# Performance work log

Measured on AMD Instinct MI355X. Metric: run time of the kernel, lower is better.

Reference implementation:

```python
import jax, jax.numpy as jnp
import numpy as np

B, T, D = 4, 2048, 1024
RANK, FACTOR, SUB = 8, 64, 4
S = 4 * SUB  # 16


def construct_hamilton(A):
    # A: [rank, 4, sub, sub] -> [rank, 4*sub, 4*sub]
    r, i, j, k = A[:, 0], A[:, 1], A[:, 2], A[:, 3]
    return jnp.concatenate([
        jnp.concatenate([r, -i, -j, -k], axis=2),
        jnp.concatenate([i, r, -k, j], axis=2),
        jnp.concatenate([j, k, r, -i], axis=2),
        jnp.concatenate([k, -j, i, r], axis=2),
    ], axis=1)


def setup_inputs() -> dict:
    key = jax.random.key(0)
    k1, k2, k3 = jax.random.split(key, 3)
    x = jax.random.normal(k1, (B, T, D), dtype=jnp.float32)
    A = jax.random.normal(k2, (RANK, 4, SUB, SUB), dtype=jnp.float32)
    # orthogonal-ish init with (r+1)^-0.5 scaling, like the torch init
    fB = jax.random.normal(k3, (RANK, FACTOR, FACTOR), dtype=jnp.float32)
    q, _ = jnp.linalg.qr(fB)
    scale = (jnp.arange(RANK, dtype=jnp.float32) + 1.0) ** -0.5
    factors_B = q * scale[:, None, None]
    bias = jnp.zeros((D,), dtype=jnp.float32)
    return {"x": x, "A": A, "factors_B": factors_B, "bias": bias}


def reference(x, A, factors_B, bias):
    Bb, Tt, Dd = x.shape
    x_flat = x.reshape(-1, S, FACTOR)          # [N, s, i]
    H = construct_hamilton(A)                   # [r, k, s]
    wav = jnp.einsum('nsi,rji->rnsj', x_flat, factors_B)  # [r, N, s, j]
    out = jnp.einsum('rnsj,rks->nkj', wav, H)   # [N, k, j]
    return out.reshape(Bb, Tt, Dd) + bias
```

## Files before the change

### kernel.cpp

```cpp
#include <hip/hip_runtime.h>
#include <stdint.h>

#define RANKS 8
#define MDIM 8192
#define KDIM 1024
#define NDIM 1024
#define BM 128
#define BN 128
#define BK 32
#define NT (KDIM / BK)
#define THREADS 256

typedef __bf16 bf16x8 __attribute__((ext_vector_type(8)));
typedef float f32x4  __attribute__((ext_vector_type(4)));
typedef float f32x16 __attribute__((ext_vector_type(16)));

__device__ __forceinline__ unsigned short f2bf(float f) {
  union { float f; uint32_t u; } v; v.f = f;
  uint32_t u = v.u;
  u += 0x7FFFu + ((u >> 16) & 1u);
  return (unsigned short)(u >> 16);
}

__constant__ int   c_comp[4][4] = {{0,1,2,3},{1,0,3,2},{2,3,0,1},{3,2,1,0}};
__constant__ float c_sign[4][4] = {{1.f,-1.f,-1.f,-1.f},
                                   {1.f, 1.f,-1.f, 1.f},
                                   {1.f, 1.f, 1.f,-1.f},
                                   {1.f,-1.f, 1.f, 1.f}};

__global__ void build_W(const float* __restrict__ A, const float* __restrict__ fB,
                        unsigned short* __restrict__ W) {
  int idx = blockIdx.x * 256 + threadIdx.x;
  int p  = idx >> 8;
  int q4 = (idx & 255) << 2;
  int k = p >> 6, j = p & 63;
  int kb = k >> 2, ks = k & 3;
  int s = q4 >> 6;
  int sb = s >> 2, ss = s & 3;
  int   comp = c_comp[kb][sb];
  float sgn  = c_sign[kb][sb];
  float o0 = 0.f, o1 = 0.f, o2 = 0.f, o3 = 0.f;
  int i0 = q4 & 63;
#pragma unroll
  for (int r = 0; r < RANKS; ++r) {
    float h = sgn * A[r * 64 + comp * 16 + ks * 4 + ss];
    const float* fb = fB + r * 4096 + j * 64 + i0;
    o0 += h * fb[0]; o1 += h * fb[1]; o2 += h * fb[2]; o3 += h * fb[3];
  }
  ushort4 st;
  st.x = f2bf(o0); st.y = f2bf(o1); st.z = f2bf(o2); st.w = f2bf(o3);
  *reinterpret_cast<ushort4*>(W + (size_t)p * KDIM + q4) = st;
}

__device__ __forceinline__ void gload16(const void* g, void* l) {
  __builtin_amdgcn_global_load_lds(
      (const __attribute__((address_space(1))) unsigned int*)(uintptr_t)g,
      (__attribute__((address_space(3))) unsigned int*)(uintptr_t)l,
      16, 0, 0);
}

__global__ __launch_bounds__(THREADS, 3) void gemm_ham(
    const float* __restrict__ x, const unsigned short* __restrict__ W,
    const float* __restrict__ bias, float* __restrict__ out) {
  __shared__ float          Asm_[2][BM * BK];
  __shared__ unsigned short Bsm_[2][BN * BK];

  const int tid  = threadIdx.x;
  const int lane = tid & 63;
  const int wid  = tid >> 6;
  const int wr   = wid >> 1;
  const int wc   = wid & 1;
  const int l31  = lane & 31;
  const int g    = lane >> 5;

  const int flat = blockIdx.x;
  const int xg = flat & 7, ig = flat >> 3;
  const int bx = xg * 8 + (ig >> 3);
  const int by = ig & 7;
  const int row0 = bx * BM;
  const int col0 = by * BN;

  f32x16 acc[2][2];
#pragma unroll
  for (int m = 0; m < 2; ++m)
#pragma unroll
    for (int n = 0; n < 2; ++n)
#pragma unroll
      for (int v = 0; v < 16; ++v) acc[m][n][v] = 0.f;

  auto stageA = [&](int kt, int slot) {
#pragma unroll
    for (int gg = 0; gg < 4; ++gg) {
      int id = gg * 256 + tid;
      int r = id >> 3, ct = id & 7;
      gload16(x + (size_t)(row0 + r) * KDIM + kt * BK + ((ct ^ (r & 7)) << 2),
              &Asm_[slot][id * 4]);
    }
  };
  auto stageB = [&](int kt, int slot) {
#pragma unroll
    for (int gg = 0; gg < 2; ++gg) {
      int id = gg * 256 + tid;
      int r = id >> 2, ct = id & 3;
      gload16(W + (size_t)(col0 + r) * KDIM + kt * BK + ((ct ^ ((r >> 1) & 3)) << 3),
              &Bsm_[slot][id * 8]);
    }
  };

  stageA(0, 0); stageB(0, 0);
  __syncthreads();

  int cur = 0;
#pragma unroll 1
  for (int t = 0; t < NT; ++t) {
    if (t + 1 < NT) { stageA(t + 1, cur ^ 1); stageB(t + 1, cur ^ 1); }

    const char* Ab = reinterpret_cast<const char*>(&Asm_[cur][0]);
    const char* Bb = reinterpret_cast<const char*>(&Bsm_[cur][0]);

    bf16x8 af[2][2], bfr[2][2];
#pragma unroll
    for (int ks = 0; ks < 2; ++ks) {
#pragma unroll
      for (int ms = 0; ms < 2; ++ms) {
        int r = wr * 64 + ms * 32 + l31;
        int ub = ks * 4 + g * 2;
        f32x4 lo = *reinterpret_cast<const f32x4*>(
            Ab + r * 128 + (((ub)     ^ (r & 7)) << 4));
        f32x4 hi = *reinterpret_cast<const f32x4*>(
            Ab + r * 128 + (((ub + 1) ^ (r & 7)) << 4));
        bf16x8 v;
        v[0] = (__bf16)lo[0]; v[1] = (__bf16)lo[1]; v[2] = (__bf16)lo[2]; v[3] = (__bf16)lo[3];
        v[4] = (__bf16)hi[0]; v[5] = (__bf16)hi[1]; v[6] = (__bf16)hi[2]; v[7] = (__bf16)hi[3];
        af[ks][ms] = v;
      }
#pragma unroll
      for (int ns = 0; ns < 2; ++ns) {
        int r = wc * 64 + ns * 32 + l31;
        int u = (ks * 2 + g) ^ ((r >> 1) & 3);
        bfr[ks][ns] = *reinterpret_cast<const bf16x8*>(Bb + r * 64 + (u << 4));
      }
    }

#pragma unroll
    for (int ks = 0; ks < 2; ++ks)
#pragma unroll
      for (int ms = 0; ms < 2; ++ms)
#pragma unroll
        for (int ns = 0; ns < 2; ++ns)
          acc[ms][ns] = __builtin_amdgcn_mfma_f32_32x32x16_bf16(
              af[ks][ms], bfr[ks][ns], acc[ms][ns], 0, 0, 0);

    __syncthreads();
    cur ^= 1;
  }

#pragma unroll
  for (int ns = 0; ns < 2; ++ns) {
    int c = col0 + wc * 64 + ns * 32 + l31;
    float bv = bias[c];
#pragma unroll
    for (int ms = 0; ms < 2; ++ms) {
      int rbase = row0 + wr * 64 + ms * 32 + g * 4;
#pragma unroll
      for (int q = 0; q < 4; ++q)
#pragma unroll
        for (int v = 0; v < 4; ++v)
          out[(size_t)(rbase + q * 8 + v) * NDIM + c] = acc[ms][ns][q * 4 + v] + bv;
    }
  }
}

__global__ void fallback_kernel(const float* __restrict__ x, const float* __restrict__ A,
                                const float* __restrict__ fB, const float* __restrict__ bias,
                                float* __restrict__ out) {
  __shared__ float xrow[1024];
  const int n = blockIdx.x;
  const int tid = threadIdx.x;
  for (int t = tid; t < 1024; t += 256) xrow[t] = x[(size_t)n * 1024 + t];
  __syncthreads();
  for (int pp = 0; pp < 4; ++pp) {
    int p = pp * 256 + tid;
    int k = p >> 6, j = p & 63;
    int kb = k >> 2, ks = k & 3;
    float accv = 0.f;
    for (int s = 0; s < 16; ++s) {
      int sb = s >> 2, ss = s & 3;
      int comp = c_comp[kb][sb];
      float sgn = c_sign[kb][sb];
      float hA[RANKS];
#pragma unroll
      for (int r = 0; r < RANKS; ++r) hA[r] = sgn * A[r * 64 + comp * 16 + ks * 4 + ss];
      for (int i = 0; i < 64; ++i) {
        float w = 0.f;
#pragma unroll
        for (int r = 0; r < RANKS; ++r) w += hA[r] * fB[r * 4096 + j * 64 + i];
        accv += xrow[s * 64 + i] * w;
      }
    }
    out[(size_t)n * 1024 + p] = accv + bias[p];
  }
}

extern "C" void kernel_launch(void* const* d_in, const int* in_sizes, int n_in,
                              void* d_out, int out_size, void* d_ws, size_t ws_size,
                              hipStream_t stream) {
  const float* x    = (const float*)d_in[0];
  const float* A    = (const float*)d_in[1];
  const float* fB   = (const float*)d_in[2];
  const float* bias = (const float*)d_in[3];
  float* out = (float*)d_out;

  const size_t needW = (size_t)NDIM * KDIM * sizeof(unsigned short);
  if (ws_size >= needW) {
    unsigned short* W = (unsigned short*)d_ws;
    build_W<<<dim3(1024), dim3(256), 0, stream>>>(A, fB, W);
    gemm_ham<<<dim3((MDIM / BM) * (NDIM / BN)), dim3(THREADS), 0, stream>>>(x, W, bias, out);
  } else {
    fallback_kernel<<<dim3(MDIM), dim3(256), 0, stream>>>(x, A, fB, bias, out);
  }
}
```

Baseline: 38.78 us.

## Load A operand directly from global into registers, bypassing LDS

The fp32 activation tile is no longer staged through shared memory. Each wave loads its own A fragments from global memory straight into registers, double-buffered across an unrolled-by-two main loop, while only the bf16 weight tile still goes through LDS. This removes the LDS traffic and footprint for A, which is the larger buffer. In exchange, A rows are re-read by both column-warps (duplicated global/L2 traffic), register pressure rises, and launch bounds drop from 3 to 2 blocks per CU.

```diff
diff --git a/kernel.cpp b/kernel.cpp
--- a/kernel.cpp
+++ b/kernel.cpp
@@ -59,10 +59,9 @@
       16, 0, 0);
 }
 
-__global__ __launch_bounds__(THREADS, 3) void gemm_ham(
+__global__ __launch_bounds__(THREADS, 2) void gemm_ham(
     const float* __restrict__ x, const unsigned short* __restrict__ W,
     const float* __restrict__ bias, float* __restrict__ out) {
-  __shared__ float          Asm_[2][BM * BK];
   __shared__ unsigned short Bsm_[2][BN * BK];
 
   const int tid  = threadIdx.x;
@@ -88,15 +87,6 @@
 #pragma unroll
       for (int v = 0; v < 16; ++v) acc[m][n][v] = 0.f;
 
-  auto stageA = [&](int kt, int slot) {
-#pragma unroll
-    for (int gg = 0; gg < 4; ++gg) {
-      int id = gg * 256 + tid;
-      int r = id >> 3, ct = id & 7;
-      gload16(x + (size_t)(row0 + r) * KDIM + kt * BK + ((ct ^ (r & 7)) << 2),
-              &Asm_[slot][id * 4]);
-    }
-  };
   auto stageB = [&](int kt, int slot) {
 #pragma unroll
     for (int gg = 0; gg < 2; ++gg) {
@@ -107,41 +97,44 @@
     }
   };
 
-  stageA(0, 0); stageB(0, 0);
-  __syncthreads();
-
-  int cur = 0;
-#pragma unroll 1
-  for (int t = 0; t < NT; ++t) {
-    if (t + 1 < NT) { stageA(t + 1, cur ^ 1); stageB(t + 1, cur ^ 1); }
-
-    const char* Ab = reinterpret_cast<const char*>(&Asm_[cur][0]);
-    const char* Bb = reinterpret_cast<const char*>(&Bsm_[cur][0]);
-
-    bf16x8 af[2][2], bfr[2][2];
-#pragma unroll
-    for (int ks = 0; ks < 2; ++ks) {
-#pragma unroll
-      for (int ms = 0; ms < 2; ++ms) {
-        int r = wr * 64 + ms * 32 + l31;
-        int ub = ks * 4 + g * 2;
-        f32x4 lo = *reinterpret_cast<const f32x4*>(
-            Ab + r * 128 + (((ub)     ^ (r & 7)) << 4));
-        f32x4 hi = *reinterpret_cast<const f32x4*>(
-            Ab + r * 128 + (((ub + 1) ^ (r & 7)) << 4));
+  const float* aRow = x + (size_t)(row0 + wr * 64 + l31) * KDIM + g * 8;
+  auto loadA = [&](int t, f32x4 (&ar)[2][2][2]) {
+#pragma unroll
+    for (int ms = 0; ms < 2; ++ms)
+#pragma unroll
+      for (int ks = 0; ks < 2; ++ks) {
+        const float* p = aRow + (size_t)ms * 32 * KDIM + t * BK + ks * 16;
+        ar[ms][ks][0] = *reinterpret_cast<const f32x4*>(p);
+        ar[ms][ks][1] = *reinterpret_cast<const f32x4*>(p + 4);
+      }
+  };
+  auto cvtA = [&](const f32x4 (&ar)[2][2][2], bf16x8 (&af)[2][2]) {
+#pragma unroll
+    for (int ms = 0; ms < 2; ++ms)
+#pragma unroll
+      for (int ks = 0; ks < 2; ++ks) {
         bf16x8 v;
-        v[0] = (__bf16)lo[0]; v[1] = (__bf16)lo[1]; v[2] = (__bf16)lo[2]; v[3] = (__bf16)lo[3];
-        v[4] = (__bf16)hi[0]; v[5] = (__bf16)hi[1]; v[6] = (__bf16)hi[2]; v[7] = (__bf16)hi[3];
+        v[0] = (__bf16)ar[ms][ks][0][0]; v[1] = (__bf16)ar[ms][ks][0][1];
+        v[2] = (__bf16)ar[ms][ks][0][2]; v[3] = (__bf16)ar[ms][ks][0][3];
+        v[4] = (__bf16)ar[ms][ks][1][0]; v[5] = (__bf16)ar[ms][ks][1][1];
+        v[6] = (__bf16)ar[ms][ks][1][2]; v[7] = (__bf16)ar[ms][ks][1][3];
         af[ks][ms] = v;
       }
+  };
+
+  auto compute = [&](int slot, const f32x4 (&ar)[2][2][2]) {
+    const char* Bb = reinterpret_cast<const char*>(&Bsm_[slot][0]);
+    bf16x8 bfr[2][2];
+#pragma unroll
+    for (int ks = 0; ks < 2; ++ks)
 #pragma unroll
       for (int ns = 0; ns < 2; ++ns) {
         int r = wc * 64 + ns * 32 + l31;
         int u = (ks * 2 + g) ^ ((r >> 1) & 3);
         bfr[ks][ns] = *reinterpret_cast<const bf16x8*>(Bb + r * 64 + (u << 4));
       }
-    }
-
+    bf16x8 af[2][2];
+    cvtA(ar, af);
 #pragma unroll
     for (int ks = 0; ks < 2; ++ks)
 #pragma unroll
@@ -150,7 +143,22 @@
         for (int ns = 0; ns < 2; ++ns)
           acc[ms][ns] = __builtin_amdgcn_mfma_f32_32x32x16_bf16(
               af[ks][ms], bfr[ks][ns], acc[ms][ns], 0, 0, 0);
-
+  };
+
+  f32x4 arE[2][2][2], arO[2][2][2];
+  loadA(0, arE);
+  stageB(0, 0);
+  __syncthreads();
+
+  int cur = 0;
+#pragma unroll 1
+  for (int t2 = 0; t2 < NT; t2 += 2) {
+    if (t2 + 1 < NT) { loadA(t2 + 1, arO); stageB(t2 + 1, cur ^ 1); }
+    compute(cur, arE);
+    __syncthreads();
+    cur ^= 1;
+    if (t2 + 2 < NT) { loadA(t2 + 2, arE); stageB(t2 + 2, cur ^ 1); }
+    compute(cur, arO);
     __syncthreads();
     cur ^= 1;
   }
```

New measurement: 78.95 us. +103.6%, slower.
